# Optimization experiments

Hardware: AMD Instinct MI355X
Metric: run time of the kernel (lower is better)

## Reference

```python
import jax, jax.numpy as jnp
import numpy as np

K = 8        # neighborhood kernel size (ksize)
HEADS = 8
GROUPS = 32  # GroupNorm groups
EPS = 1e-6
DIL = 1      # dilation


def _nbr_idx(L, k, d):
    # NATTEN-style neighborhood: fixed-size window, shifted (clamped) at borders
    span = (k - 1) * d + 1
    i = jnp.arange(L)
    start = jnp.clip(i - ((k - 1) // 2) * d, 0, L - span)
    return start[:, None] + jnp.arange(k)[None, :] * d  # [L, k]


def _group_norm(x, gamma, beta):
    B, C, H, W = x.shape
    xg = x.reshape(B, GROUPS, C // GROUPS, H, W)
    mu = xg.mean(axis=(2, 3, 4), keepdims=True)
    var = xg.var(axis=(2, 3, 4), keepdims=True)
    xn = ((xg - mu) * jax.lax.rsqrt(var + EPS)).reshape(B, C, H, W)
    return xn * gamma[None, :, None, None] + beta[None, :, None, None]


def setup_inputs() -> dict:
    key = jax.random.key(0)
    ks = jax.random.split(key, 4)
    B, C, H, W = 2, 128, 96, 96
    x = jax.random.normal(ks[0], (B, C, H, W), dtype=jnp.float32)
    gn_gamma = jnp.ones((C,), jnp.float32)
    gn_beta = jnp.zeros((C,), jnp.float32)
    qkv_w = jax.random.normal(ks[1], (3 * C, C), dtype=jnp.float32) * (C ** -0.5)
    qkv_b = jnp.zeros((3 * C,), jnp.float32)
    proj_w = jax.random.normal(ks[2], (C, C), dtype=jnp.float32) * (C ** -0.5)
    proj_b = jnp.zeros((C,), jnp.float32)
    return {"x": x, "gn_gamma": gn_gamma, "gn_beta": gn_beta,
            "qkv_w": qkv_w, "qkv_b": qkv_b, "proj_w": proj_w, "proj_b": proj_b}


def reference(x, gn_gamma, gn_beta, qkv_w, qkv_b, proj_w, proj_b):
    B, C, H, W = x.shape
    hd = C // HEADS
    h = _group_norm(x, gn_gamma, gn_beta)
    # 1x1 conv -> qkv
    qkv = jnp.einsum('bchw,oc->bohw', h, qkv_w) + qkv_b[None, :, None, None]
    # 'b (qkv h c) x y -> qkv b x y h c'
    qkv = qkv.reshape(B, 3, HEADS, hd, H, W).transpose(1, 0, 4, 5, 2, 3)
    q, k, v = qkv[0], qkv[1], qkv[2]  # [B,H,W,heads,hd]

    ih = _nbr_idx(H, K, DIL)  # [H,K]
    iw = _nbr_idx(W, K, DIL)  # [W,K]
    # gather per-pixel K x K neighborhoods -> [B,H,W,K,K,heads,hd]
    k_win = k[:, ih[:, None, :, None], iw[None, :, None, :]]
    v_win = v[:, ih[:, None, :, None], iw[None, :, None, :]]

    scale = np.float32(1.0 / np.sqrt(hd))
    logits = jnp.einsum('bxyhc,bxyijhc->bxyhij', q * scale, k_win)
    logits = logits.reshape(B, H, W, HEADS, K * K)
    attn = jax.nn.softmax(logits, axis=-1)
    out = jnp.einsum('bxyhm,bxymhc->bxyhc', attn,
                     v_win.reshape(B, H, W, K * K, HEADS, hd))
    # 'b x y h c -> b (h c) x y'
    out = out.transpose(0, 3, 4, 1, 2).reshape(B, C, H, W)
    return jnp.einsum('bchw,oc->bohw', out, proj_w) + proj_b[None, :, None, None]
```

## Files before the change

### kernel.cpp

```cpp
#include <hip/hip_runtime.h>
#include <hip/hip_bf16.h>

typedef unsigned short u16;
typedef unsigned int   u32;
typedef __attribute__((ext_vector_type(8))) short short8;
typedef __attribute__((ext_vector_type(4))) float f32x4;

#define BATCH 2
#define CCH   128
#define HH    96
#define WW    96
#define HWSZ  9216
#define HEADS 8
#define HD    16
#define GROUPS 32
#define EPSV  1e-6f

static __device__ __forceinline__ u16 f2bf(float f) {
    u32 u = __builtin_bit_cast(u32, f);
    u = (u + 0x7FFFu + ((u >> 16) & 1u)) >> 16;
    return (u16)u;
}
static __device__ __forceinline__ short8 mk8(u32 a, u32 b, u32 c, u32 d) {
    union { short8 v; u32 w[4]; } u; u.w[0]=a; u.w[1]=b; u.w[2]=c; u.w[3]=d; return u.v;
}

__global__ __launch_bounds__(256) void gn_wpack(const float* __restrict__ x,
                                                float* __restrict__ partial,
                                                const float* __restrict__ qkv_w,
                                                const float* __restrict__ proj_w,
                                                u16* __restrict__ Wq, u16* __restrict__ Wp) {
    if (blockIdx.x < 256) {
        const int bq = blockIdx.x;
        const float4* base = (const float4*)(x + (size_t)bq * 9216);
        float s = 0.f, ss = 0.f;
        #pragma unroll
        for (int i = 0; i < 9; ++i) {
            float4 v = base[threadIdx.x + i * 256];
            s  += v.x + v.y + v.z + v.w;
            ss += v.x * v.x + v.y * v.y + v.z * v.z + v.w * v.w;
        }
        #pragma unroll
        for (int off = 32; off > 0; off >>= 1) {
            s  += __shfl_down(s, off);
            ss += __shfl_down(ss, off);
        }
        __shared__ float rs[4], rss[4];
        const int wid = threadIdx.x >> 6, lane = threadIdx.x & 63;
        if (lane == 0) { rs[wid] = s; rss[wid] = ss; }
        __syncthreads();
        if (threadIdx.x == 0) {
            partial[2 * bq]     = rs[0] + rs[1] + rs[2] + rs[3];
            partial[2 * bq + 1] = rss[0] + rss[1] + rss[2] + rss[3];
        }
    } else {
        const int t = (blockIdx.x - 256) * 256 + threadIdx.x;
        if (t < 16 * 384) {
            int cb = t / 384, o = t % 384;
            u16 pk[8];
            #pragma unroll
            for (int j = 0; j < 8; ++j) pk[j] = f2bf(qkv_w[o * 128 + cb * 8 + j]);
            uint4 r;
            r.x = (u32)pk[0] | ((u32)pk[1] << 16); r.y = (u32)pk[2] | ((u32)pk[3] << 16);
            r.z = (u32)pk[4] | ((u32)pk[5] << 16); r.w = (u32)pk[6] | ((u32)pk[7] << 16);
            *(uint4*)(Wq + (size_t)t * 8) = r;
        } else if (t < 16 * 384 + 16 * 128) {
            int i = t - 16 * 384;
            int cb = i / 128, o = i % 128;
            u16 pk[8];
            #pragma unroll
            for (int j = 0; j < 8; ++j) pk[j] = f2bf(proj_w[o * 128 + cb * 8 + j]);
            uint4 r;
            r.x = (u32)pk[0] | ((u32)pk[1] << 16); r.y = (u32)pk[2] | ((u32)pk[3] << 16);
            r.z = (u32)pk[4] | ((u32)pk[5] << 16); r.w = (u32)pk[6] | ((u32)pk[7] << 16);
            *(uint4*)(Wp + (size_t)i * 8) = r;
        }
    }
}

__global__ __launch_bounds__(256) void qkv_fused(const float* __restrict__ x,
                                                 const float* __restrict__ partial,
                                                 const float* __restrict__ gamma,
                                                 const float* __restrict__ beta,
                                                 const u16* __restrict__ Wq,
                                                 const float* __restrict__ qkv_b,
                                                 u16* __restrict__ qkvp,
                                                 u16* __restrict__ vT) {
    __shared__ float scale[CCH], shift[CCH];
    __shared__ u16 Xt[16][128][8];
    const int t = threadIdx.x;
    const int pph = blockIdx.x;
    const int L = (pph & 7) * 54 + (pph >> 3);
    const int b = L / 216;
    const int r = L % 216;
    const int pt = r / 3, ot = r % 3;

    if (t < CCH) {
        const int c = t, g = c >> 2, bg = b * GROUPS + g;
        float S = 0.f, SS = 0.f;
        #pragma unroll
        for (int q = 0; q < 4; ++q) {
            S  += partial[2 * (bg * 4 + q)];
            SS += partial[2 * (bg * 4 + q) + 1];
        }
        const float mean = S * (1.f / 36864.f);
        const float rstd = rsqrtf(SS * (1.f / 36864.f) - mean * mean + EPSV);
        const float sc = rstd * gamma[c];
        scale[c] = sc;
        shift[c] = beta[c] - mean * sc;
    }
    __syncthreads();

    {
        const int px = t & 127, chh = t >> 7;
        const float* xb = x + (size_t)b * CCH * HWSZ + (size_t)pt * 128 + px;
        #pragma unroll
        for (int cbi = 0; cbi < 8; ++cbi) {
            const int cb = chh * 8 + cbi;
            u16 pk[8];
            #pragma unroll
            for (int j = 0; j < 8; ++j) {
                const int c = cb * 8 + j;
                pk[j] = f2bf(xb[(size_t)c * HWSZ] * scale[c] + shift[c]);
            }
            uint4 o;
            o.x = (u32)pk[0] | ((u32)pk[1] << 16);
            o.y = (u32)pk[2] | ((u32)pk[3] << 16);
            o.z = (u32)pk[4] | ((u32)pk[5] << 16);
            o.w = (u32)pk[6] | ((u32)pk[7] << 16);
            *(uint4*)&Xt[cb][px][0] = o;
        }
    }
    __syncthreads();

    const int l = t & 63, w = t >> 6;
    const int OB = ot * 128 + (w & 1) * 64;
    const int PL = (w >> 1) * 64;
    const int q = l >> 4, lo = l & 15;

    float bv[4][4];
    #pragma unroll
    for (int of = 0; of < 4; ++of)
        #pragma unroll
        for (int r2 = 0; r2 < 4; ++r2) bv[of][r2] = qkv_b[OB + of * 16 + q * 4 + r2];

    f32x4 acc[4][4] = {};
    #pragma unroll
    for (int ks = 0; ks < 4; ++ks) {
        const int cb = ks * 4 + q;
        short8 a[4];
        #pragma unroll
        for (int of = 0; of < 4; ++of)
            a[of] = *(const short8*)(Wq + ((size_t)cb * 384 + OB + of * 16 + lo) * 8);
        #pragma unroll
        for (int pf = 0; pf < 4; ++pf) {
            short8 bb = *(const short8*)&Xt[cb][PL + pf * 16 + lo][0];
            #pragma unroll
            for (int of = 0; of < 4; ++of)
                acc[of][pf] = __builtin_amdgcn_mfma_f32_16x16x32_bf16(a[of], bb, acc[of][pf], 0, 0, 0);
        }
    }

    #pragma unroll
    for (int of = 0; of < 4; ++of) {
        const int pl = (OB >> 4) + of;
        if (pl < 16) {
            const int plane = b * 16 + pl;
            #pragma unroll
            for (int pf = 0; pf < 4; ++pf) {
                const int p = pt * 128 + PL + pf * 16 + lo;
                u16 h0 = f2bf(acc[of][pf][0] + bv[of][0]);
                u16 h1 = f2bf(acc[of][pf][1] + bv[of][1]);
                u16 h2 = f2bf(acc[of][pf][2] + bv[of][2]);
                u16 h3 = f2bf(acc[of][pf][3] + bv[of][3]);
                uint2 pkt;
                pkt.x = (u32)h0 | ((u32)h1 << 16);
                pkt.y = (u32)h2 | ((u32)h3 << 16);
                *(uint2*)(qkvp + ((size_t)plane * HWSZ + p) * 16 + q * 4) = pkt;
            }
        } else {
            const int h = pl - 16;
            #pragma unroll
            for (int pf = 0; pf < 4; ++pf) {
                const int p = pt * 128 + PL + pf * 16 + lo;
                #pragma unroll
                for (int r2 = 0; r2 < 4; ++r2)
                    vT[(((size_t)(b * 8 + h)) * 16 + q * 4 + r2) * HWSZ + p] =
                        f2bf(acc[of][pf][r2] + bv[of][r2]);
            }
        }
    }
}

template<int MTOT>
__global__ __launch_bounds__(256) void proj_gemm(const u16* __restrict__ Wpk,
                                                 const u16* __restrict__ Xpk,
                                                 const float* __restrict__ bias,
                                                 float* __restrict__ out_f32) {
    const int l = threadIdx.x & 63, w = threadIdx.x >> 6;
    const int pt = blockIdx.x, ot = blockIdx.y, b = blockIdx.z;
    const int OB = ot * 128 + (w & 1) * 64;
    const int PB = pt * 128 + (w >> 1) * 64;
    const int q = l >> 4, lo = l & 15;
    const u16* Xb = Xpk + (size_t)b * 16 * HWSZ * 8;

    float bv[4][4];
    #pragma unroll
    for (int of = 0; of < 4; ++of)
        #pragma unroll
        for (int r = 0; r < 4; ++r) bv[of][r] = bias[OB + of * 16 + q * 4 + r];

    f32x4 acc[4][4] = {};
    #pragma unroll
    for (int ks = 0; ks < 4; ++ks) {
        const int cb = ks * 4 + q;
        short8 a[4];
        #pragma unroll
        for (int of = 0; of < 4; ++of)
            a[of] = *(const short8*)(Wpk + ((size_t)cb * MTOT + OB + of * 16 + lo) * 8);
        #pragma unroll
        for (int pf = 0; pf < 4; ++pf) {
            short8 bb = *(const short8*)(Xb + ((size_t)cb * HWSZ + PB + pf * 16 + lo) * 8);
            #pragma unroll
            for (int of = 0; of < 4; ++of)
                acc[of][pf] = __builtin_amdgcn_mfma_f32_16x16x32_bf16(a[of], bb, acc[of][pf], 0, 0, 0);
        }
    }

    #pragma unroll
    for (int of = 0; of < 4; ++of) {
        #pragma unroll
        for (int pf = 0; pf < 4; ++pf) {
            const int p = PB + pf * 16 + lo;
            #pragma unroll
            for (int r = 0; r < 4; ++r) {
                const int o = OB + of * 16 + q * 4 + r;
                out_f32[((size_t)(b * MTOT + o)) * HWSZ + p] = acc[of][pf][r] + bv[of][r];
            }
        }
    }
}

__global__ __launch_bounds__(384) void natten_mfma(const u16* __restrict__ qkv,
                                                   const u16* __restrict__ vT,
                                                   u16* __restrict__ attn_out) {
    __shared__ u16 Ks[13 * 64 * 16];
    __shared__ u16 VsT[16 * 840];
    const int tid = threadIdx.x;
    const int xh = blockIdx.x & 1, yb = blockIdx.x >> 1;
    const int h = blockIdx.y, b = blockIdx.z;
    const int ry0 = min(max(yb * 6 - 3, 0), 83);
    const int rx0 = xh * 32;

    for (int i = tid; i < 3328; i += 384) {
        if (i < 1664) {
            const int px = i >> 1, half = i & 1;
            const int row = px >> 6, col = px & 63;
            const u16* gp = qkv + ((size_t)(b * 16 + 8 + h) * HWSZ
                                 + (ry0 + row) * WW + rx0 + col) * 16 + half * 8;
            *(uint4*)&Ks[px * 16 + half * 8] = *(const uint4*)gp;
        } else {
            const int j2 = i - 1664;
            const int ch = j2 / 104, r2 = j2 - ch * 104;
            const int row = r2 >> 3, c8 = r2 & 7;
            const u16* gp = vT + (((size_t)(b * 8 + h)) * 16 + ch) * HWSZ
                               + (ry0 + row) * WW + rx0 + c8 * 8;
            *(uint4*)&VsT[ch * 840 + row * 64 + c8 * 8] = *(const uint4*)gp;
        }
    }
    __syncthreads();

    const int l = tid & 63, wv = tid >> 6;
    const int m = l & 15, q4 = l >> 4;
    const int yq = m >> 3, xq = m & 7;

    for (int j = 0; j < 3; ++j) {
        const int g = wv * 3 + j;
        const int gy = g / 6, gx = g % 6;
        const int y0g = yb * 6 + gy * 2, x0g = xh * 48 + gx * 8;
        const int yabs = y0g + yq, xabs = x0g + xq;
        const int sy = min(max(yabs - 3, 0), 88);
        const int sx = min(max(xabs - 3, 0), 88);
        const int dy0 = min(max(y0g - 3, 0), 88) - ry0;
        const int rd0 = dy0 - (sy - ry0);
        const int cx0 = (min(max(x0g - 3 - rx0, 0), 48)) & ~3;
        const int cd0 = cx0 + q4 * 4 - (sx - rx0);
        const int qpix = yabs * WW + xabs;

        const uint2 qw = *(const uint2*)(qkv + ((size_t)(b * 16 + h) * HWSZ + qpix) * 16 + q4 * 4);
        const short8 qb = mk8(qw.x, qw.y, 0u, 0u);

        float ev[9][4];
        float vs = 0.f;
        #pragma unroll
        for (int t = 0; t < 9; ++t) {
            const int trow = min(dy0 + t, 12);
            const uint2 kk = *(const uint2*)&Ks[(trow * 64 + cx0 + m) * 16 + q4 * 4];
            f32x4 lg = __builtin_amdgcn_mfma_f32_16x16x32_bf16(
                mk8(kk.x, kk.y, kk.x, kk.y), qb, (f32x4){0.f, 0.f, 0.f, 0.f}, 0, 0, 0);
            const bool rv = (u32)(t + rd0) < 8u;
            #pragma unroll
            for (int r = 0; r < 4; ++r) {
                const bool ok = rv && ((u32)(cd0 + r) < 8u);
                const float e = ok ? __expf(lg[r] * 0.25f) : 0.f;
                ev[t][r] = e;
                vs += e;
            }
        }
        vs += __shfl_xor(vs, 16);
        vs += __shfl_xor(vs, 32);
        const float inv = 1.0f / vs;

        u32 pd0[9], pd1[9];
        #pragma unroll
        for (int t = 0; t < 9; ++t) {
            pd0[t] = (u32)f2bf(ev[t][0] * inv) | ((u32)f2bf(ev[t][1] * inv) << 16);
            pd1[t] = (u32)f2bf(ev[t][2] * inv) | ((u32)f2bf(ev[t][3] * inv) << 16);
        }

        f32x4 acc = {};
        #pragma unroll
        for (int t = 0; t < 9; ++t) {
            const int trow = min(dy0 + t, 12);
            const uint2 va = *(const uint2*)&VsT[m * 840 + trow * 64 + cx0 + q4 * 4];
            acc = __builtin_amdgcn_mfma_f32_16x16x32_bf16(
                mk8(va.x, va.y, va.x, va.y), mk8(pd0[t], pd1[t], 0u, 0u), acc, 0, 0, 0);
        }

        uint2 od;
        od.x = (u32)f2bf(acc[0]) | ((u32)f2bf(acc[1]) << 16);
        od.y = (u32)f2bf(acc[2]) | ((u32)f2bf(acc[3]) << 16);
        *(uint2*)(attn_out + ((size_t)(b * 16 + h * 2 + (q4 >> 1)) * HWSZ + qpix) * 8
                  + (q4 & 1) * 4) = od;
    }
}

extern "C" void kernel_launch(void* const* d_in, const int* in_sizes, int n_in,
                              void* d_out, int out_size, void* d_ws, size_t ws_size,
                              hipStream_t stream) {
    const float* x      = (const float*)d_in[0];
    const float* gamma  = (const float*)d_in[1];
    const float* beta   = (const float*)d_in[2];
    const float* qkv_w  = (const float*)d_in[3];
    const float* qkv_b  = (const float*)d_in[4];
    const float* proj_w = (const float*)d_in[5];
    const float* proj_b = (const float*)d_in[6];
    float* out = (float*)d_out;

    char* wsb = (char*)d_ws;
    float* partial = (float*)wsb;
    u16* Wq    = (u16*)(wsb + 4096);
    u16* Wp    = Wq + 16 * 384 * 8;
    u16* qkvp  = Wp + 16 * 128 * 8;
    u16* vT    = qkvp + (size_t)BATCH * 16 * HWSZ * HD;
    u16* attnp = vT + (size_t)BATCH * 8 * HD * HWSZ;

    gn_wpack<<<288, 256, 0, stream>>>(x, partial, qkv_w, proj_w, Wq, Wp);

    qkv_fused<<<432, 256, 0, stream>>>(x, partial, gamma, beta, Wq, qkv_b, qkvp, vT);

    natten_mfma<<<dim3(32, HEADS, BATCH), 384, 0, stream>>>(qkvp, vT, attnp);

    proj_gemm<128><<<dim3(HWSZ / 128, 1, BATCH), 256, 0, stream>>>(
        Wp, attnp, proj_b, out);
}
```

Baseline: 44.58 us.

## Stage V transpose through LDS for coalesced stores and halve proj_gemm tile

In qkv_fused, blocks that produce V now write results into a padded shared buffer that reuses the Xt storage, then emit 16-byte coalesced rows to vT instead of scattered 2-byte stores. proj_gemm drops its template and uses a 64-pixel tile per block, launching 288 blocks instead of 144 so more CUs are busy. The costs are extra barriers in the V blocks and half as much weight reuse per block in the projection.

Result: faster. 43.15 us (-3.2%).

```diff
diff --git a/kernel.cpp b/kernel.cpp
--- a/kernel.cpp
+++ b/kernel.cpp
@@ -87,7 +87,7 @@
                                                  u16* __restrict__ qkvp,
                                                  u16* __restrict__ vT) {
     __shared__ float scale[CCH], shift[CCH];
-    __shared__ u16 Xt[16][128][8];
+    __shared__ u16 smem[128 * 136];
     const int t = threadIdx.x;
     const int pph = blockIdx.x;
     const int L = (pph & 7) * 54 + (pph >> 3);
@@ -128,7 +128,7 @@
             o.y = (u32)pk[2] | ((u32)pk[3] << 16);
             o.z = (u32)pk[4] | ((u32)pk[5] << 16);
             o.w = (u32)pk[6] | ((u32)pk[7] << 16);
-            *(uint4*)&Xt[cb][px][0] = o;
+            *(uint4*)&smem[((size_t)cb * 128 + px) * 8] = o;
         }
     }
     __syncthreads();
@@ -154,18 +154,17 @@
             a[of] = *(const short8*)(Wq + ((size_t)cb * 384 + OB + of * 16 + lo) * 8);
         #pragma unroll
         for (int pf = 0; pf < 4; ++pf) {
-            short8 bb = *(const short8*)&Xt[cb][PL + pf * 16 + lo][0];
+            short8 bb = *(const short8*)&smem[((size_t)cb * 128 + PL + pf * 16 + lo) * 8];
             #pragma unroll
             for (int of = 0; of < 4; ++of)
                 acc[of][pf] = __builtin_amdgcn_mfma_f32_16x16x32_bf16(a[of], bb, acc[of][pf], 0, 0, 0);
         }
     }
 
-    #pragma unroll
-    for (int of = 0; of < 4; ++of) {
-        const int pl = (OB >> 4) + of;
-        if (pl < 16) {
-            const int plane = b * 16 + pl;
+    if (ot < 2) {
+        #pragma unroll
+        for (int of = 0; of < 4; ++of) {
+            const int plane = b * 16 + (OB >> 4) + of;
             #pragma unroll
             for (int pf = 0; pf < 4; ++pf) {
                 const int p = pt * 128 + PL + pf * 16 + lo;
@@ -178,29 +177,42 @@
                 pkt.y = (u32)h2 | ((u32)h3 << 16);
                 *(uint2*)(qkvp + ((size_t)plane * HWSZ + p) * 16 + q * 4) = pkt;
             }
-        } else {
-            const int h = pl - 16;
+        }
+    } else {
+        __syncthreads();
+        #pragma unroll
+        for (int of = 0; of < 4; ++of) {
+            const int orow = (OB - 256) + of * 16 + q * 4;
             #pragma unroll
             for (int pf = 0; pf < 4; ++pf) {
-                const int p = pt * 128 + PL + pf * 16 + lo;
+                const int px = PL + pf * 16 + lo;
                 #pragma unroll
                 for (int r2 = 0; r2 < 4; ++r2)
-                    vT[(((size_t)(b * 8 + h)) * 16 + q * 4 + r2) * HWSZ + p] =
-                        f2bf(acc[of][pf][r2] + bv[of][r2]);
-            }
-        }
-    }
-}
-
-template<int MTOT>
+                    smem[(orow + r2) * 136 + px] = f2bf(acc[of][pf][r2] + bv[of][r2]);
+            }
+        }
+        __syncthreads();
+        #pragma unroll
+        for (int k = 0; k < 8; ++k) {
+            const int idx = t + k * 256;
+            const int row = idx >> 4, px8 = idx & 15;
+            const int h = row >> 4, ch = row & 15;
+            uint4 v = *(const uint4*)&smem[row * 136 + px8 * 8];
+            *(uint4*)(vT + ((((size_t)(b * 8 + h)) * 16 + ch) * HWSZ)
+                      + (size_t)pt * 128 + px8 * 8) = v;
+        }
+    }
+}
+
 __global__ __launch_bounds__(256) void proj_gemm(const u16* __restrict__ Wpk,
                                                  const u16* __restrict__ Xpk,
                                                  const float* __restrict__ bias,
                                                  float* __restrict__ out_f32) {
+    const int bid = blockIdx.x;
+    const int b = bid / 144, pt = bid % 144;
     const int l = threadIdx.x & 63, w = threadIdx.x >> 6;
-    const int pt = blockIdx.x, ot = blockIdx.y, b = blockIdx.z;
-    const int OB = ot * 128 + (w & 1) * 64;
-    const int PB = pt * 128 + (w >> 1) * 64;
+    const int OB = (w & 1) * 64;
+    const int PB = pt * 64 + (w >> 1) * 32;
     const int q = l >> 4, lo = l & 15;
     const u16* Xb = Xpk + (size_t)b * 16 * HWSZ * 8;
 
@@ -210,16 +222,16 @@
         #pragma unroll
         for (int r = 0; r < 4; ++r) bv[of][r] = bias[OB + of * 16 + q * 4 + r];
 
-    f32x4 acc[4][4] = {};
+    f32x4 acc[4][2] = {};
     #pragma unroll
     for (int ks = 0; ks < 4; ++ks) {
         const int cb = ks * 4 + q;
         short8 a[4];
         #pragma unroll
         for (int of = 0; of < 4; ++of)
-            a[of] = *(const short8*)(Wpk + ((size_t)cb * MTOT + OB + of * 16 + lo) * 8);
-        #pragma unroll
-        for (int pf = 0; pf < 4; ++pf) {
+            a[of] = *(const short8*)(Wpk + ((size_t)cb * 128 + OB + of * 16 + lo) * 8);
+        #pragma unroll
+        for (int pf = 0; pf < 2; ++pf) {
             short8 bb = *(const short8*)(Xb + ((size_t)cb * HWSZ + PB + pf * 16 + lo) * 8);
             #pragma unroll
             for (int of = 0; of < 4; ++of)
@@ -230,12 +242,12 @@
     #pragma unroll
     for (int of = 0; of < 4; ++of) {
         #pragma unroll
-        for (int pf = 0; pf < 4; ++pf) {
+        for (int pf = 0; pf < 2; ++pf) {
             const int p = PB + pf * 16 + lo;
             #pragma unroll
             for (int r = 0; r < 4; ++r) {
                 const int o = OB + of * 16 + q * 4 + r;
-                out_f32[((size_t)(b * MTOT + o)) * HWSZ + p] = acc[of][pf][r] + bv[of][r];
+                out_f32[((size_t)(b * 128 + o)) * HWSZ + p] = acc[of][pf][r] + bv[of][r];
             }
         }
     }
@@ -361,6 +373,5 @@
 
     natten_mfma<<<dim3(32, HEADS, BATCH), 384, 0, stream>>>(qkvp, vT, attnp);
 
-    proj_gemm<128><<<dim3(HWSZ / 128, 1, BATCH), 256, 0, stream>>>(
-        Wp, attnp, proj_b, out);
-}
+    proj_gemm<<<288, 256, 0, stream>>>(Wp, attnp, proj_b, out);
+}
```
